# Optimization experiments

Measured on AMD Instinct MI355X. Metric: run time of the kernel, lower is better.

## Reference

```python
import jax, jax.numpy as jnp
import numpy as np

N_NODES, N_FEAT, HIDDEN, N_CLASSES, N_EDGES = 100000, 64, 64, 16, 1600000


def setup_inputs() -> dict:
    key = jax.random.key(0)
    ks = jax.random.split(key, 10)
    x = jax.random.normal(ks[0], (N_NODES, N_FEAT), dtype=jnp.float32)
    edge_index = jax.random.randint(ks[1], (2, N_EDGES), 0, N_NODES, dtype=jnp.int32)
    edge_weight = jax.random.uniform(ks[2], (N_EDGES,), dtype=jnp.float32)
    # Glorot-style init for GCNConv weights, zero bias (as in torch_geometric)
    W1 = jax.random.normal(ks[3], (N_FEAT, HIDDEN), dtype=jnp.float32) / np.float32(np.sqrt(N_FEAT))
    b1 = jnp.zeros((HIDDEN,), jnp.float32)
    W2 = jax.random.normal(ks[4], (HIDDEN, HIDDEN), dtype=jnp.float32) / np.float32(np.sqrt(HIDDEN))
    b2 = jnp.zeros((HIDDEN,), jnp.float32)
    W3 = jax.random.normal(ks[5], (HIDDEN, N_CLASSES), dtype=jnp.float32) / np.float32(np.sqrt(HIDDEN))
    b3 = jnp.zeros((N_CLASSES,), jnp.float32)
    return {"x": x, "edge_index": edge_index, "edge_weight": edge_weight,
            "W1": W1, "b1": b1, "W2": W2, "b2": b2, "W3": W3, "b3": b3}


def _gcn_norm(edge_index, edge_weight, num_nodes):
    """Add self-loops (weight 1) and compute symmetric D^-1/2 A D^-1/2 norm."""
    loop = jnp.arange(num_nodes, dtype=edge_index.dtype)
    src = jnp.concatenate([edge_index[0], loop])
    dst = jnp.concatenate([edge_index[1], loop])
    ew = jnp.concatenate([edge_weight, jnp.ones((num_nodes,), edge_weight.dtype)])
    deg = jax.ops.segment_sum(ew, dst, num_segments=num_nodes)
    dis = jnp.where(deg > 0, jax.lax.rsqrt(jnp.where(deg > 0, deg, 1.0)), 0.0)
    norm = dis[src] * ew * dis[dst]  # [E+N]
    return src, dst, norm


def reference(x, edge_index, edge_weight, W1, b1, W2, b2, W3, b3):
    N = x.shape[0]
    src, dst, norm = _gcn_norm(edge_index, edge_weight, N)

    def conv(h, W, b):
        hw = h @ W                                   # [N, out]
        msg = norm[:, None] * hw[src]                # [E+N, out]
        return jax.ops.segment_sum(msg, dst, num_segments=N) + b

    # conv1 + ReLU (dropout is identity in eval mode)
    h = jax.nn.relu(conv(x, W1, b1))
    # one hidden GCNConv layer (num_layer=3)
    h = jax.nn.relu(conv(h, W2, b2))
    logits = conv(h, W3, b3)                         # [N, C]
    out = jax.nn.log_softmax(logits, axis=1)
    return (out, logits, logits)
```

## Files before the change

### kernel.cpp

```cpp
#include <hip/hip_runtime.h>
#include <hip/hip_bf16.h>

#define N_FEAT 64
#define NBW 9
#define SRC_BITS 23
#define CAP 9216

typedef unsigned short u16;
typedef __attribute__((ext_vector_type(8))) short short8;
typedef __attribute__((ext_vector_type(4))) float f32x4;

__device__ inline u16 f2bf(float f) {
    unsigned u = __float_as_uint(f);
    u += 0x7fffu + ((u >> 16) & 1u);
    return (u16)(u >> 16);
}


__device__ inline void packW(const float* __restrict__ W, uint4* __restrict__ Wpk,
                             int ncb, int wcols, int tid) {
    int nf = ncb * 2 * 64;
    for (int f = tid; f < nf; f += 256) {
        int cb = f >> 7;
        int s  = (f >> 6) & 1;
        int lane = f & 63;
        int kb = lane >> 4, c16 = lane & 15;
        union { uint4 q; u16 u[8]; } pk;
        #pragma unroll
        for (int i = 0; i < 8; ++i) {
            int k = s * 32 + kb * 8 + i;
            pk.u[i] = f2bf(W[k * wcols + cb * 16 + c16]);
        }
        Wpk[f] = pk.q;
    }
}

__global__ __launch_bounds__(256) void pack_init(const float* __restrict__ W1, const float* __restrict__ W2,
                                                 const float* __restrict__ W3,
                                                 uint4* Wp1, uint4* Wp2, uint4* Wp3, int* bcur) {
    if (blockIdx.x == 0)      packW(W1, Wp1, 4, 64, threadIdx.x);
    else if (blockIdx.x == 1) packW(W2, Wp2, 4, 64, threadIdx.x);
    else if (blockIdx.x == 2) packW(W3, Wp3, 1, 16, threadIdx.x);
    else                      bcur[threadIdx.x] = 0;
}


template<int OUTW, bool INBF, bool SCALE>
__device__ inline void gemm_body(const void* __restrict__ Av, const uint4* __restrict__ Wpk,
                                 const float* __restrict__ dis, u16* __restrict__ C, int N,
                                 int wid, int lane) {
    constexpr int NCB = OUTW / 16;
    int r0 = wid * 16;
    if (r0 >= N) return;
    int row16 = lane & 15, kb = lane >> 4;
    int r = min(r0 + row16, N - 1);

    short8 a0, a1;
    if (INBF) {
        const u16* arow = (const u16*)Av + (size_t)r * 64 + kb * 8;
        a0 = __builtin_bit_cast(short8, *(const uint4*)arow);
        a1 = __builtin_bit_cast(short8, *(const uint4*)(arow + 32));
    } else {
        const float* arow = (const float*)Av + (size_t)r * 64 + kb * 8;
        float4 f0 = *(const float4*)arow;
        float4 f1 = *(const float4*)(arow + 4);
        float4 f2 = *(const float4*)(arow + 32);
        float4 f3 = *(const float4*)(arow + 36);
        union { short8 v; u16 u[8]; } pa, pb;
        pa.u[0] = f2bf(f0.x); pa.u[1] = f2bf(f0.y); pa.u[2] = f2bf(f0.z); pa.u[3] = f2bf(f0.w);
        pa.u[4] = f2bf(f1.x); pa.u[5] = f2bf(f1.y); pa.u[6] = f2bf(f1.z); pa.u[7] = f2bf(f1.w);
        pb.u[0] = f2bf(f2.x); pb.u[1] = f2bf(f2.y); pb.u[2] = f2bf(f2.z); pb.u[3] = f2bf(f2.w);
        pb.u[4] = f2bf(f3.x); pb.u[5] = f2bf(f3.y); pb.u[6] = f2bf(f3.z); pb.u[7] = f2bf(f3.w);
        a0 = pa.v; a1 = pb.v;
    }

    f32x4 acc[NCB];
    #pragma unroll
    for (int cb = 0; cb < NCB; ++cb) {
        short8 b0 = __builtin_bit_cast(short8, Wpk[(cb * 2 + 0) * 64 + lane]);
        short8 b1 = __builtin_bit_cast(short8, Wpk[(cb * 2 + 1) * 64 + lane]);
        f32x4 z = {0.f, 0.f, 0.f, 0.f};
        z = __builtin_amdgcn_mfma_f32_16x16x32_bf16(a0, b0, z, 0, 0, 0);
        z = __builtin_amdgcn_mfma_f32_16x16x32_bf16(a1, b1, z, 0, 0, 0);
        acc[cb] = z;
    }

    int rbase = r0 + kb * 4;
    float dsc[4];
    #pragma unroll
    for (int j = 0; j < 4; ++j) dsc[j] = SCALE ? dis[min(rbase + j, N - 1)] : 1.0f;

    #pragma unroll
    for (int cb = 0; cb < NCB; ++cb) {
        int col = cb * 16 + row16;
        #pragma unroll
        for (int j = 0; j < 4; ++j) {
            int rr = rbase + j;
            if (rr < N) C[(size_t)rr * OUTW + col] = f2bf(SCALE ? acc[cb][j] * dsc[j] : acc[cb][j]);
        }
    }
}

template<int OUTW, bool INBF, bool SCALE>
__global__ __launch_bounds__(256) void gemm_mf(const void* __restrict__ Av, const uint4* __restrict__ Wpk,
                                               const float* __restrict__ dis,
                                               u16* __restrict__ C, int N) {
    int lane = threadIdx.x & 63;
    int wid  = (int)((blockIdx.x * blockDim.x + threadIdx.x) >> 6);
    gemm_body<OUTW, INBF, SCALE>(Av, Wpk, dis, C, N, wid, lane);
}


__global__ __launch_bounds__(256) void part_gemm(const int* __restrict__ ei, const float* __restrict__ ew,
                                                 int* bcur, int2* __restrict__ ebuf, int E, int NB, int PB,
                                                 const float* __restrict__ x, const uint4* __restrict__ Wp1,
                                                 u16* __restrict__ hwB, int N) {
    constexpr int EPT = 8;
    __shared__ int cnt[256];
    __shared__ int base[256];
    int tid = threadIdx.x;

    if ((int)blockIdx.x >= PB) {
        int wid = (int)(((blockIdx.x - PB) * blockDim.x + tid) >> 6);
        gemm_body<64, false, false>(x, Wp1, nullptr, hwB, N, wid, tid & 63);
        return;
    }

    cnt[tid] = 0;
    __syncthreads();
    int start = blockIdx.x * (256 * EPT);

    int d[EPT], r[EPT], s[EPT]; float w[EPT];
    #pragma unroll
    for (int i = 0; i < EPT; ++i) {
        int e = start + i * 256 + tid;
        if (e < E) {
            d[i] = ei[E + e];
            s[i] = ei[e];
            w[i] = ew[e];
            r[i] = atomicAdd(&cnt[d[i] >> NBW], 1);
        } else d[i] = -1;
    }
    __syncthreads();
    if (tid < NB && cnt[tid]) base[tid] = atomicAdd(&bcur[tid], cnt[tid]);
    __syncthreads();
    #pragma unroll
    for (int i = 0; i < EPT; ++i) {
        if (d[i] >= 0) {
            int b = d[i] >> NBW;
            int dl = d[i] & ((1 << NBW) - 1);
            int gpos = base[b] + r[i];
            if (gpos < CAP) {
                int key = (dl << SRC_BITS) | s[i];
                ebuf[(size_t)b * CAP + gpos] = make_int2(key, __float_as_int(w[i]));
            }
        }
    }
}


__global__ __launch_bounds__(256) void bucket_csr(const int2* __restrict__ ebuf, const int* __restrict__ bcur,
                                                  int2* __restrict__ csr, int* __restrict__ rowp,
                                                  int* __restrict__ cnt, float* __restrict__ dis, int N) {
    __shared__ int   h[512];
    __shared__ float ws[512];
    __shared__ int   off[512];
    __shared__ int   wsum[4];
    int b = blockIdx.x, tid = threadIdx.x;
    int nbase = b << NBW;
    int nn = min(512, N - nbase);
    int beg = b * CAP;
    int m = min(bcur[b], CAP);

    h[tid] = 0; h[tid + 256] = 0;
    ws[tid] = 0.f; ws[tid + 256] = 0.f;
    __syncthreads();

    for (int i = tid; i < m; i += 256) {
        int2 en = ebuf[beg + i];
        int dl = ((unsigned)en.x) >> SRC_BITS;
        atomicAdd(&h[dl], 1);
        atomicAdd(&ws[dl], __int_as_float(en.y));
    }
    __syncthreads();

    int v0 = h[2 * tid], v1 = h[2 * tid + 1];
    int v = v0 + v1;
    int lane = tid & 63, wv = tid >> 6;
    int incl = v;
    #pragma unroll
    for (int o = 1; o < 64; o <<= 1) { int t = __shfl_up(incl, o); if (lane >= o) incl += t; }
    if (lane == 63) wsum[wv] = incl;
    __syncthreads();
    int add = 0;
    #pragma unroll
    for (int i = 0; i < 4; ++i) if (i < wv) add += wsum[i];
    int excl = add + incl - v;
    off[2 * tid] = excl;
    off[2 * tid + 1] = excl + v0;
    __syncthreads();

    for (int l = tid; l < nn; l += 256) {
        rowp[nbase + l] = beg + off[l];
        cnt[nbase + l]  = h[l];
        dis[nbase + l]  = rsqrtf(1.0f + ws[l]);
    }
    __syncthreads();
    h[tid] = 0; h[tid + 256] = 0;
    __syncthreads();

    for (int i = tid; i < m; i += 256) {
        int2 en = ebuf[beg + i];
        unsigned k = (unsigned)en.x;
        int dl  = k >> SRC_BITS;
        int src = k & ((1 << SRC_BITS) - 1);
        int pos = atomicAdd(&h[dl], 1);
        csr[beg + off[dl] + pos] = make_int2(src, en.y);
    }
}


template<int F, bool RELU, bool FINAL, bool LOADDIS>
__global__ __launch_bounds__(256) void aggregate(const u16* __restrict__ hw, const int* __restrict__ rowp,
                                                 const int* __restrict__ cnt, const int2* __restrict__ csr,
                                                 const float* __restrict__ dis,
                                                 const float* __restrict__ bias, void* __restrict__ outv,
                                                 float* __restrict__ out2, float* __restrict__ out3, int N) {
    constexpr int GL   = F / 8;
    constexpr int NPW  = 64 / GL;
    constexpr unsigned ROWB = F * 2;
    constexpr int UN   = 8;

    int wv   = (int)((blockIdx.x * blockDim.x + threadIdx.x) >> 6);
    int lane = threadIdx.x & 63;
    int g = lane / GL;
    int t = lane % GL;
    int n = wv * NPW + g;
    bool alive = (n < N);
    n = min(n, N - 1);

    float dd = dis[n];
    int beg = rowp[n];
    int c   = cnt[n];
    const char* hwb = (const char*)hw;
    unsigned toff = (unsigned)t * 16u;

    float acc[8];
    {
        uint4 raw = *(const uint4*)(hwb + (unsigned)n * ROWB + toff);
        float sw = LOADDIS ? dd : 1.0f;
        unsigned uw[4] = {raw.x, raw.y, raw.z, raw.w};
        #pragma unroll
        for (int k = 0; k < 4; ++k) {
            acc[2 * k]     = sw * __uint_as_float(uw[k] << 16);
            acc[2 * k + 1] = sw * __uint_as_float(uw[k] & 0xffff0000u);
        }
    }

    for (int j0 = 0; j0 < c; j0 += UN) {
        int2 e[UN];
        #pragma unroll
        for (int i = 0; i < UN; ++i) e[i] = csr[beg + min(j0 + i, c - 1)];
        uint4 r[UN]; float w[UN];
        #pragma unroll
        for (int i = 0; i < UN; ++i) {
            r[i] = *(const uint4*)(hwb + (unsigned)e[i].x * ROWB + toff);
            float wr = __int_as_float(e[i].y);
            if (LOADDIS) wr *= dis[e[i].x];
            w[i] = (j0 + i < c) ? wr : 0.0f;
        }
        #pragma unroll
        for (int i = 0; i < UN; ++i) {
            unsigned u[4] = {r[i].x, r[i].y, r[i].z, r[i].w};
            #pragma unroll
            for (int k = 0; k < 4; ++k) {
                acc[2 * k]     = fmaf(w[i], __uint_as_float(u[k] << 16), acc[2 * k]);
                acc[2 * k + 1] = fmaf(w[i], __uint_as_float(u[k] & 0xffff0000u), acc[2 * k + 1]);
            }
        }
    }

    if (alive) {
        float4 b0 = *(const float4*)&bias[t * 8];
        float4 b1 = *(const float4*)&bias[t * 8 + 4];
        float bb[8] = {b0.x, b0.y, b0.z, b0.w, b1.x, b1.y, b1.z, b1.w};
        #pragma unroll
        for (int k = 0; k < 8; ++k) acc[k] = fmaf(dd, acc[k], bb[k]);
        if (RELU) {
            #pragma unroll
            for (int k = 0; k < 8; ++k) acc[k] = fmaxf(acc[k], 0.0f);
        }
        if (!FINAL) {
            u16* o16 = (u16*)outv;
            uint4 pk;
            pk.x = (unsigned)f2bf(acc[0]) | ((unsigned)f2bf(acc[1]) << 16);
            pk.y = (unsigned)f2bf(acc[2]) | ((unsigned)f2bf(acc[3]) << 16);
            pk.z = (unsigned)f2bf(acc[4]) | ((unsigned)f2bf(acc[5]) << 16);
            pk.w = (unsigned)f2bf(acc[6]) | ((unsigned)f2bf(acc[7]) << 16);
            *(uint4*)&o16[(size_t)n * F + t * 8] = pk;
        } else {
            float4 r0 = make_float4(acc[0], acc[1], acc[2], acc[3]);
            float4 r1 = make_float4(acc[4], acc[5], acc[6], acc[7]);
            *(float4*)&out2[(size_t)n * F + t * 8] = r0;
            *(float4*)&out2[(size_t)n * F + t * 8 + 4] = r1;
            *(float4*)&out3[(size_t)n * F + t * 8] = r0;
            *(float4*)&out3[(size_t)n * F + t * 8 + 4] = r1;
            float mloc = acc[0];
            #pragma unroll
            for (int k = 1; k < 8; ++k) mloc = fmaxf(mloc, acc[k]);
            float m = fmaxf(mloc, __shfl_xor(mloc, 1));
            float sloc = 0.f;
            #pragma unroll
            for (int k = 0; k < 8; ++k) sloc += __expf(acc[k] - m);
            float ssum = sloc + __shfl_xor(sloc, 1);
            float ls = m + __logf(ssum);
            float* o = (float*)outv;
            float4 w0 = make_float4(acc[0] - ls, acc[1] - ls, acc[2] - ls, acc[3] - ls);
            float4 w1 = make_float4(acc[4] - ls, acc[5] - ls, acc[6] - ls, acc[7] - ls);
            *(float4*)&o[(size_t)n * F + t * 8] = w0;
            *(float4*)&o[(size_t)n * F + t * 8 + 4] = w1;
        }
    }
}


extern "C" void kernel_launch(void* const* d_in, const int* in_sizes, int n_in,
                              void* d_out, int out_size, void* d_ws, size_t ws_size,
                              hipStream_t stream) {
    const float* x   = (const float*)d_in[0];
    const int*   ei  = (const int*)d_in[1];
    const float* ew  = (const float*)d_in[2];
    const float* W1  = (const float*)d_in[3];
    const float* b1  = (const float*)d_in[4];
    const float* W2  = (const float*)d_in[5];
    const float* b2  = (const float*)d_in[6];
    const float* W3  = (const float*)d_in[7];
    const float* b3  = (const float*)d_in[8];
    float* out = (float*)d_out;

    const int N = in_sizes[0] / N_FEAT;
    const int E = in_sizes[2];
    const int NB = (N + (1 << NBW) - 1) >> NBW;

    size_t off = 0;
    auto alloc = [&](size_t bytes) {
        void* p = (char*)d_ws + off;
        off += (bytes + 255) & ~(size_t)255;
        return p;
    };
    float* dis     = (float*)alloc((size_t)N * 4);
    int*   cnt     = (int*)alloc((size_t)N * 4);
    int*   rowp    = (int*)alloc((size_t)N * 4);
    int*   bcur    = (int*)alloc(256 * 4);
    int2*  csr     = (int2*)alloc((size_t)NB * CAP * 8);
    int2*  ebuf    = (int2*)alloc((size_t)NB * CAP * 8);
    u16*   bufA16  = (u16*)alloc((size_t)N * 64 * 2);
    u16*   hwB     = (u16*)alloc((size_t)N * 64 * 2);
    u16*   hw16    = (u16*)alloc((size_t)N * 16 * 2);
    uint4* Wp1     = (uint4*)alloc(512 * 16);
    uint4* Wp2     = (uint4*)alloc(512 * 16);
    uint4* Wp3     = (uint4*)alloc(128 * 16);

    const int TB = 256;

    int gblk = ((N + 15) / 16 + 3) / 4;
    int PB   = (E + 2047) / 2048;

    pack_init<<<4, TB, 0, stream>>>(W1, W2, W3, Wp1, Wp2, Wp3, bcur);
    part_gemm<<<PB + gblk, TB, 0, stream>>>(ei, ew, bcur, ebuf, E, NB, PB, x, Wp1, hwB, N);
    bucket_csr<<<NB, TB, 0, stream>>>(ebuf, bcur, csr, rowp, cnt, dis, N);

    int ablk64 = (N * 8 + TB - 1) / TB;
    int ablk16 = (N * 2 + TB - 1) / TB;

    float* logits = out + (size_t)N * 16;
    float* logits2 = out + (size_t)2 * N * 16;

    aggregate<64, true, false, true><<<ablk64, TB, 0, stream>>>(hwB, rowp, cnt, csr, dis, b1, bufA16, nullptr, nullptr, N);
    gemm_mf<64, true, true><<<gblk, TB, 0, stream>>>(bufA16, Wp2, dis, hwB, N);
    aggregate<64, true, false, false><<<ablk64, TB, 0, stream>>>(hwB, rowp, cnt, csr, dis, b2, bufA16, nullptr, nullptr, N);
    gemm_mf<16, true, true><<<gblk, TB, 0, stream>>>(bufA16, Wp3, dis, hw16, N);
    aggregate<16, false, true, false><<<ablk16, TB, 0, stream>>>(hw16, rowp, cnt, csr, dis, b3, out, logits, logits2, N);
}
```

Measured before the change: 175.4 us.

## Fuse aggregation with following MFMA GEMM through shared memory

Each layer's sparse aggregation now stages its ReLU'd bf16 output for 32 nodes in LDS, and two waves then run the next layer's MFMA GEMM on that tile. This replaces separate aggregate and gemm kernels and removes the global round trip of the intermediate activation buffer plus two launches. The cost is a block barrier, and only half the waves do the GEMM while the rest sit idle. The final layer gets its own specialised aggregation and log-softmax kernel.

```diff
diff --git a/kernel.cpp b/kernel.cpp
--- a/kernel.cpp
+++ b/kernel.cpp
@@ -101,15 +101,6 @@
     }
 }
 
-template<int OUTW, bool INBF, bool SCALE>
-__global__ __launch_bounds__(256) void gemm_mf(const void* __restrict__ Av, const uint4* __restrict__ Wpk,
-                                               const float* __restrict__ dis,
-                                               u16* __restrict__ C, int N) {
-    int lane = threadIdx.x & 63;
-    int wid  = (int)((blockIdx.x * blockDim.x + threadIdx.x) >> 6);
-    gemm_body<OUTW, INBF, SCALE>(Av, Wpk, dis, C, N, wid, lane);
-}
-
 
 __global__ __launch_bounds__(256) void part_gemm(const int* __restrict__ ei, const float* __restrict__ ew,
                                                  int* bcur, int2* __restrict__ ebuf, int E, int NB, int PB,
@@ -157,7 +148,6 @@
         }
     }
 }
-
 
 __global__ __launch_bounds__(256) void bucket_csr(const int2* __restrict__ ebuf, const int* __restrict__ bcur,
                                                   int2* __restrict__ csr, int* __restrict__ rowp,
@@ -220,22 +210,21 @@
 }
 
 
-template<int F, bool RELU, bool FINAL, bool LOADDIS>
-__global__ __launch_bounds__(256) void aggregate(const u16* __restrict__ hw, const int* __restrict__ rowp,
-                                                 const int* __restrict__ cnt, const int2* __restrict__ csr,
-                                                 const float* __restrict__ dis,
-                                                 const float* __restrict__ bias, void* __restrict__ outv,
-                                                 float* __restrict__ out2, float* __restrict__ out3, int N) {
-    constexpr int GL   = F / 8;
-    constexpr int NPW  = 64 / GL;
-    constexpr unsigned ROWB = F * 2;
-    constexpr int UN   = 8;
-
-    int wv   = (int)((blockIdx.x * blockDim.x + threadIdx.x) >> 6);
-    int lane = threadIdx.x & 63;
-    int g = lane / GL;
-    int t = lane % GL;
-    int n = wv * NPW + g;
+template<int OUTW, bool LOADDIS>
+__global__ __launch_bounds__(256) void agg_gemm(const u16* __restrict__ hw, const int* __restrict__ rowp,
+                                                const int* __restrict__ cnt, const int2* __restrict__ csr,
+                                                const float* __restrict__ dis, const float* __restrict__ bias,
+                                                const uint4* __restrict__ Wpk, u16* __restrict__ C, int N) {
+    constexpr int UN = 8;
+    __shared__ u16 As[32 * 64];
+
+    int tid  = threadIdx.x;
+    int w    = tid >> 6;
+    int lane = tid & 63;
+    int g = lane >> 3;
+    int t = lane & 7;
+    int l = w * 8 + g;
+    int n = blockIdx.x * 32 + l;
     bool alive = (n < N);
     n = min(n, N - 1);
 
@@ -247,7 +236,7 @@
 
     float acc[8];
     {
-        uint4 raw = *(const uint4*)(hwb + (unsigned)n * ROWB + toff);
+        uint4 raw = *(const uint4*)(hwb + (unsigned)n * 128u + toff);
         float sw = LOADDIS ? dd : 1.0f;
         unsigned uw[4] = {raw.x, raw.y, raw.z, raw.w};
         #pragma unroll
@@ -261,21 +250,126 @@
         int2 e[UN];
         #pragma unroll
         for (int i = 0; i < UN; ++i) e[i] = csr[beg + min(j0 + i, c - 1)];
-        uint4 r[UN]; float w[UN];
+        uint4 r[UN]; float wgt[UN];
         #pragma unroll
         for (int i = 0; i < UN; ++i) {
-            r[i] = *(const uint4*)(hwb + (unsigned)e[i].x * ROWB + toff);
+            r[i] = *(const uint4*)(hwb + (unsigned)e[i].x * 128u + toff);
             float wr = __int_as_float(e[i].y);
             if (LOADDIS) wr *= dis[e[i].x];
-            w[i] = (j0 + i < c) ? wr : 0.0f;
+            wgt[i] = (j0 + i < c) ? wr : 0.0f;
         }
         #pragma unroll
         for (int i = 0; i < UN; ++i) {
             unsigned u[4] = {r[i].x, r[i].y, r[i].z, r[i].w};
             #pragma unroll
             for (int k = 0; k < 4; ++k) {
-                acc[2 * k]     = fmaf(w[i], __uint_as_float(u[k] << 16), acc[2 * k]);
-                acc[2 * k + 1] = fmaf(w[i], __uint_as_float(u[k] & 0xffff0000u), acc[2 * k + 1]);
+                acc[2 * k]     = fmaf(wgt[i], __uint_as_float(u[k] << 16), acc[2 * k]);
+                acc[2 * k + 1] = fmaf(wgt[i], __uint_as_float(u[k] & 0xffff0000u), acc[2 * k + 1]);
+            }
+        }
+    }
+
+    {
+        float4 b0 = *(const float4*)&bias[t * 8];
+        float4 b1 = *(const float4*)&bias[t * 8 + 4];
+        float bb[8] = {b0.x, b0.y, b0.z, b0.w, b1.x, b1.y, b1.z, b1.w};
+        #pragma unroll
+        for (int k = 0; k < 8; ++k) acc[k] = fmaxf(fmaf(dd, acc[k], bb[k]), 0.0f);
+        uint4 pk;
+        pk.x = (unsigned)f2bf(acc[0]) | ((unsigned)f2bf(acc[1]) << 16);
+        pk.y = (unsigned)f2bf(acc[2]) | ((unsigned)f2bf(acc[3]) << 16);
+        pk.z = (unsigned)f2bf(acc[4]) | ((unsigned)f2bf(acc[5]) << 16);
+        pk.w = (unsigned)f2bf(acc[6]) | ((unsigned)f2bf(acc[7]) << 16);
+        *(uint4*)&As[l * 64 + t * 8] = pk;
+    }
+    __syncthreads();
+
+    if (w < 2) {
+        constexpr int NCB = OUTW / 16;
+        int r0 = blockIdx.x * 32 + w * 16;
+        if (r0 < N) {
+            int row16 = lane & 15, kb = lane >> 4;
+            const u16* arow = &As[(w * 16 + row16) * 64 + kb * 8];
+            short8 a0 = __builtin_bit_cast(short8, *(const uint4*)arow);
+            short8 a1 = __builtin_bit_cast(short8, *(const uint4*)(arow + 32));
+
+            f32x4 za[NCB];
+            #pragma unroll
+            for (int cb = 0; cb < NCB; ++cb) {
+                short8 b0 = __builtin_bit_cast(short8, Wpk[(cb * 2 + 0) * 64 + lane]);
+                short8 b1 = __builtin_bit_cast(short8, Wpk[(cb * 2 + 1) * 64 + lane]);
+                f32x4 z = {0.f, 0.f, 0.f, 0.f};
+                z = __builtin_amdgcn_mfma_f32_16x16x32_bf16(a0, b0, z, 0, 0, 0);
+                z = __builtin_amdgcn_mfma_f32_16x16x32_bf16(a1, b1, z, 0, 0, 0);
+                za[cb] = z;
+            }
+
+            int rbase = r0 + kb * 4;
+            float dsc[4];
+            #pragma unroll
+            for (int j = 0; j < 4; ++j) dsc[j] = dis[min(rbase + j, N - 1)];
+            #pragma unroll
+            for (int cb = 0; cb < NCB; ++cb) {
+                int col = cb * 16 + row16;
+                #pragma unroll
+                for (int j = 0; j < 4; ++j) {
+                    int rr = rbase + j;
+                    if (rr < N) C[(size_t)rr * OUTW + col] = f2bf(za[cb][j] * dsc[j]);
+                }
+            }
+        }
+    }
+}
+
+
+__global__ __launch_bounds__(256) void agg_final(const u16* __restrict__ hw, const int* __restrict__ rowp,
+                                                 const int* __restrict__ cnt, const int2* __restrict__ csr,
+                                                 const float* __restrict__ dis, const float* __restrict__ bias,
+                                                 float* __restrict__ out0, float* __restrict__ out2,
+                                                 float* __restrict__ out3, int N) {
+    constexpr int UN = 8;
+    int wv   = (int)((blockIdx.x * blockDim.x + threadIdx.x) >> 6);
+    int lane = threadIdx.x & 63;
+    int g = lane >> 1;
+    int t = lane & 1;
+    int n = wv * 32 + g;
+    bool alive = (n < N);
+    n = min(n, N - 1);
+
+    float dd = dis[n];
+    int beg = rowp[n];
+    int c   = cnt[n];
+    const char* hwb = (const char*)hw;
+    unsigned toff = (unsigned)t * 16u;
+
+    float acc[8];
+    {
+        uint4 raw = *(const uint4*)(hwb + (unsigned)n * 32u + toff);
+        unsigned uw[4] = {raw.x, raw.y, raw.z, raw.w};
+        #pragma unroll
+        for (int k = 0; k < 4; ++k) {
+            acc[2 * k]     = __uint_as_float(uw[k] << 16);
+            acc[2 * k + 1] = __uint_as_float(uw[k] & 0xffff0000u);
+        }
+    }
+
+    for (int j0 = 0; j0 < c; j0 += UN) {
+        int2 e[UN];
+        #pragma unroll
+        for (int i = 0; i < UN; ++i) e[i] = csr[beg + min(j0 + i, c - 1)];
+        uint4 r[UN]; float wgt[UN];
+        #pragma unroll
+        for (int i = 0; i < UN; ++i) {
+            r[i] = *(const uint4*)(hwb + (unsigned)e[i].x * 32u + toff);
+            wgt[i] = (j0 + i < c) ? __int_as_float(e[i].y) : 0.0f;
+        }
+        #pragma unroll
+        for (int i = 0; i < UN; ++i) {
+            unsigned u[4] = {r[i].x, r[i].y, r[i].z, r[i].w};
+            #pragma unroll
+            for (int k = 0; k < 4; ++k) {
+                acc[2 * k]     = fmaf(wgt[i], __uint_as_float(u[k] << 16), acc[2 * k]);
+                acc[2 * k + 1] = fmaf(wgt[i], __uint_as_float(u[k] & 0xffff0000u), acc[2 * k + 1]);
             }
         }
     }
@@ -286,40 +380,26 @@
         float bb[8] = {b0.x, b0.y, b0.z, b0.w, b1.x, b1.y, b1.z, b1.w};
         #pragma unroll
         for (int k = 0; k < 8; ++k) acc[k] = fmaf(dd, acc[k], bb[k]);
-        if (RELU) {
-            #pragma unroll
-            for (int k = 0; k < 8; ++k) acc[k] = fmaxf(acc[k], 0.0f);
-        }
-        if (!FINAL) {
-            u16* o16 = (u16*)outv;
-            uint4 pk;
-            pk.x = (unsigned)f2bf(acc[0]) | ((unsigned)f2bf(acc[1]) << 16);
-            pk.y = (unsigned)f2bf(acc[2]) | ((unsigned)f2bf(acc[3]) << 16);
-            pk.z = (unsigned)f2bf(acc[4]) | ((unsigned)f2bf(acc[5]) << 16);
-            pk.w = (unsigned)f2bf(acc[6]) | ((unsigned)f2bf(acc[7]) << 16);
-            *(uint4*)&o16[(size_t)n * F + t * 8] = pk;
-        } else {
-            float4 r0 = make_float4(acc[0], acc[1], acc[2], acc[3]);
-            float4 r1 = make_float4(acc[4], acc[5], acc[6], acc[7]);
-            *(float4*)&out2[(size_t)n * F + t * 8] = r0;
-            *(float4*)&out2[(size_t)n * F + t * 8 + 4] = r1;
-            *(float4*)&out3[(size_t)n * F + t * 8] = r0;
-            *(float4*)&out3[(size_t)n * F + t * 8 + 4] = r1;
-            float mloc = acc[0];
-            #pragma unroll
-            for (int k = 1; k < 8; ++k) mloc = fmaxf(mloc, acc[k]);
-            float m = fmaxf(mloc, __shfl_xor(mloc, 1));
-            float sloc = 0.f;
-            #pragma unroll
-            for (int k = 0; k < 8; ++k) sloc += __expf(acc[k] - m);
-            float ssum = sloc + __shfl_xor(sloc, 1);
-            float ls = m + __logf(ssum);
-            float* o = (float*)outv;
-            float4 w0 = make_float4(acc[0] - ls, acc[1] - ls, acc[2] - ls, acc[3] - ls);
-            float4 w1 = make_float4(acc[4] - ls, acc[5] - ls, acc[6] - ls, acc[7] - ls);
-            *(float4*)&o[(size_t)n * F + t * 8] = w0;
-            *(float4*)&o[(size_t)n * F + t * 8 + 4] = w1;
-        }
+
+        float4 r0 = make_float4(acc[0], acc[1], acc[2], acc[3]);
+        float4 r1 = make_float4(acc[4], acc[5], acc[6], acc[7]);
+        *(float4*)&out2[(size_t)n * 16 + t * 8] = r0;
+        *(float4*)&out2[(size_t)n * 16 + t * 8 + 4] = r1;
+        *(float4*)&out3[(size_t)n * 16 + t * 8] = r0;
+        *(float4*)&out3[(size_t)n * 16 + t * 8 + 4] = r1;
+        float mloc = acc[0];
+        #pragma unroll
+        for (int k = 1; k < 8; ++k) mloc = fmaxf(mloc, acc[k]);
+        float m = fmaxf(mloc, __shfl_xor(mloc, 1));
+        float sloc = 0.f;
+        #pragma unroll
+        for (int k = 0; k < 8; ++k) sloc += __expf(acc[k] - m);
+        float ssum = sloc + __shfl_xor(sloc, 1);
+        float ls = m + __logf(ssum);
+        float4 w0 = make_float4(acc[0] - ls, acc[1] - ls, acc[2] - ls, acc[3] - ls);
+        float4 w1 = make_float4(acc[4] - ls, acc[5] - ls, acc[6] - ls, acc[7] - ls);
+        *(float4*)&out0[(size_t)n * 16 + t * 8] = w0;
+        *(float4*)&out0[(size_t)n * 16 + t * 8 + 4] = w1;
     }
 }
 
@@ -354,8 +434,8 @@
     int*   bcur    = (int*)alloc(256 * 4);
     int2*  csr     = (int2*)alloc((size_t)NB * CAP * 8);
     int2*  ebuf    = (int2*)alloc((size_t)NB * CAP * 8);
-    u16*   bufA16  = (u16*)alloc((size_t)N * 64 * 2);
     u16*   hwB     = (u16*)alloc((size_t)N * 64 * 2);
+    u16*   hwB2    = (u16*)alloc((size_t)N * 64 * 2);
     u16*   hw16    = (u16*)alloc((size_t)N * 16 * 2);
     uint4* Wp1     = (uint4*)alloc(512 * 16);
     uint4* Wp2     = (uint4*)alloc(512 * 16);
@@ -365,20 +445,17 @@
 
     int gblk = ((N + 15) / 16 + 3) / 4;
     int PB   = (E + 2047) / 2048;
+    int fblk = (N + 31) / 32;
+    int ablk16 = (N * 2 + TB - 1) / TB;
+
+    float* logits = out + (size_t)N * 16;
+    float* logits2 = out + (size_t)2 * N * 16;
 
     pack_init<<<4, TB, 0, stream>>>(W1, W2, W3, Wp1, Wp2, Wp3, bcur);
     part_gemm<<<PB + gblk, TB, 0, stream>>>(ei, ew, bcur, ebuf, E, NB, PB, x, Wp1, hwB, N);
     bucket_csr<<<NB, TB, 0, stream>>>(ebuf, bcur, csr, rowp, cnt, dis, N);
 
-    int ablk64 = (N * 8 + TB - 1) / TB;
-    int ablk16 = (N * 2 + TB - 1) / TB;
-
-    float* logits = out + (size_t)N * 16;
-    float* logits2 = out + (size_t)2 * N * 16;
-
-    aggregate<64, true, false, true><<<ablk64, TB, 0, stream>>>(hwB, rowp, cnt, csr, dis, b1, bufA16, nullptr, nullptr, N);
-    gemm_mf<64, true, true><<<gblk, TB, 0, stream>>>(bufA16, Wp2, dis, hwB, N);
-    aggregate<64, true, false, false><<<ablk64, TB, 0, stream>>>(hwB, rowp, cnt, csr, dis, b2, bufA16, nullptr, nullptr, N);
-    gemm_mf<16, true, true><<<gblk, TB, 0, stream>>>(bufA16, Wp3, dis, hw16, N);
-    aggregate<16, false, true, false><<<ablk16, TB, 0, stream>>>(hw16, rowp, cnt, csr, dis, b3, out, logits, logits2, N);
-}
+    agg_gemm<64, true><<<fblk, TB, 0, stream>>>(hwB, rowp, cnt, csr, dis, b1, Wp2, hwB2, N);
+    agg_gemm<16, false><<<fblk, TB, 0, stream>>>(hwB2, rowp, cnt, csr, dis, b2, Wp3, hw16, N);
+    agg_final<<<ablk16, TB, 0, stream>>>(hw16, rowp, cnt, csr, dis, b3, out, logits, logits2, N);
+}
```

Result: faster. 168.3 us (-4.0%).
